# Optimization experiments

Hardware: AMD Instinct MI355X
Metric: run time of the kernel (lower is better)

The kernel has to match this reference:

```python
import jax, jax.numpy as jnp
import numpy as np

N, E, IN, HID, HEADS, OUT, G = 30000, 480000, 256, 64, 8, 128, 512
NEG_SLOPE = 0.2


def setup_inputs() -> dict:
    key = jax.random.key(0)
    ks = jax.random.split(key, 20)
    def nrm(k, shape, scale=0.05):
        return jax.random.normal(k, shape, dtype=jnp.float32) * scale
    inp = {
        'x': jax.random.normal(ks[0], (N, IN), dtype=jnp.float32),
        'edge_index': jax.random.randint(ks[1], (2, E), 0, N, dtype=jnp.int32),
        'batch': jnp.sort(jax.random.randint(ks[2], (N,), 0, G, dtype=jnp.int32)),
        # conv1: in=IN, out=HID, heads=HEADS (concat)
        'W1': nrm(ks[3], (IN, HEADS * HID)),
        'a_src1': nrm(ks[4], (HEADS, HID)),
        'a_dst1': nrm(ks[5], (HEADS, HID)),
        'b1': jnp.zeros((HEADS * HID,), jnp.float32),
        # conv2: in=HEADS*HID, out=HID, heads=HEADS (concat)
        'W2': nrm(ks[6], (HEADS * HID, HEADS * HID)),
        'a_src2': nrm(ks[7], (HEADS, HID)),
        'a_dst2': nrm(ks[8], (HEADS, HID)),
        'b2': jnp.zeros((HEADS * HID,), jnp.float32),
        # conv3: in=HEADS*HID, out=HID, heads=1
        'W3': nrm(ks[9], (HEADS * HID, HID)),
        'a_src3': nrm(ks[10], (1, HID)),
        'a_dst3': nrm(ks[11], (1, HID)),
        'b3': jnp.zeros((HID,), jnp.float32),
        # fc
        'Wfc': nrm(ks[12], (HID, OUT)),
        'bfc': jnp.zeros((OUT,), jnp.float32),
    }
    return inp


def gat_conv(x, W, a_src, a_dst, b, src, dst, heads, ch):
    # x: [N, in] -> h: [N, heads, ch]
    h = (x @ W).reshape(N, heads, ch)
    alpha_s = jnp.einsum('nhc,hc->nh', h, a_src)  # [N,H]
    alpha_d = jnp.einsum('nhc,hc->nh', h, a_dst)
    e = jax.nn.leaky_relu(alpha_s[src] + alpha_d[dst], NEG_SLOPE)  # [E',H]
    # segment softmax over incoming edges of each dst node
    e = e - jax.ops.segment_max(e, dst, num_segments=N)[dst]
    e = jnp.exp(e)
    alpha = e / jax.ops.segment_sum(e, dst, num_segments=N)[dst]
    msg = h[src] * alpha[:, :, None]                   # [E',H,C]
    out = jax.ops.segment_sum(msg, dst, num_segments=N)  # [N,H,C]
    return out.reshape(N, heads * ch) + b


def reference(x, edge_index, batch, W1, a_src1, a_dst1, b1, W2, a_src2, a_dst2, b2,
              W3, a_src3, a_dst3, b3, Wfc, bfc):
    # PyG GATConv adds self-loops
    loops = jnp.arange(N, dtype=edge_index.dtype)
    src = jnp.concatenate([edge_index[0], loops])
    dst = jnp.concatenate([edge_index[1], loops])

    h = jax.nn.elu(gat_conv(x, W1, a_src1, a_dst1, b1, src, dst, HEADS, HID))
    h = jax.nn.elu(gat_conv(h, W2, a_src2, a_dst2, b2, src, dst, HEADS, HID))
    h = jax.nn.elu(gat_conv(h, W3, a_src3, a_dst3, b3, src, dst, 1, HID))

    # global mean pool over graphs
    sums = jax.ops.segment_sum(h, batch, num_segments=G)          # [G,HID]
    cnt = jax.ops.segment_sum(jnp.ones((N,), h.dtype), batch, num_segments=G)
    pooled = sums / jnp.maximum(cnt, 1.0)[:, None]
    # dropout(p=0.5) is identity in eval mode
    return pooled @ Wfc + bfc  # [G, OUT]
```

## Files before the change

kernel.cpp:

```cpp
#include <hip/hip_runtime.h>
#include <hip/hip_fp16.h>
#include <math.h>

#define N_NODES 30000
#define N_EDGES 480000
#define N_EDGES_SL (N_EDGES + N_NODES)
#define DIM_IN 256
#define F1 512
#define HEADS 8
#define NGRAPH 512
#define NEG 0.2f
#define MB_TILES 235
#define NB_SCAN 118

typedef __attribute__((ext_vector_type(8))) short short8;
typedef __attribute__((ext_vector_type(8))) _Float16 half8;
typedef __attribute__((ext_vector_type(4))) float f32x4;

__device__ __forceinline__ float lrelu(float x) { return fmaxf(x, NEG * x); }
__device__ __forceinline__ float elu_(float x) { return x > 0.f ? x : __expf(x) - 1.f; }

__device__ __forceinline__ void glds16(const unsigned short* g, unsigned short* l) {
    __builtin_amdgcn_global_load_lds(
        (const __attribute__((address_space(1))) unsigned int*)g,
        (__attribute__((address_space(3))) unsigned int*)l, 16, 0, 0);
}

__global__ __launch_bounds__(256) void k_bsum(const int* __restrict__ deg,
                                              int* __restrict__ bsum) {
    int i = blockIdx.x * 256 + threadIdx.x;
    int v = (i < N_NODES) ? deg[i] + 1 : 0;
#pragma unroll
    for (int off = 1; off < 64; off <<= 1) v += __shfl_xor(v, off);
    __shared__ int ws[4];
    if ((threadIdx.x & 63) == 0) ws[threadIdx.x >> 6] = v;
    __syncthreads();
    if (threadIdx.x == 0) bsum[blockIdx.x] = ws[0] + ws[1] + ws[2] + ws[3];
}

__global__ __launch_bounds__(128) void k_bscan(const int* __restrict__ bsum,
                                               int* __restrict__ bbase,
                                               int* __restrict__ offsN) {
    __shared__ int p[128];
    int t = threadIdx.x;
    int v = (t < NB_SCAN) ? bsum[t] : 0;
    p[t] = v;
    __syncthreads();
    for (int off = 1; off < 128; off <<= 1) {
        int x = (t >= off) ? p[t - off] : 0;
        __syncthreads();
        p[t] += x;
        __syncthreads();
    }
    if (t < NB_SCAN) bbase[t] = p[t] - v;
    if (t == 127) *offsN = p[127];
}

__global__ __launch_bounds__(256) void k_offs(const int* __restrict__ deg,
                                              const int* __restrict__ bbase,
                                              int* __restrict__ offs,
                                              int* __restrict__ cursor) {
    int b = blockIdx.x, t = threadIdx.x;
    int i = b * 256 + t;
    int v = (i < N_NODES) ? deg[i] + 1 : 0;
    __shared__ int p[256];
    p[t] = v;
    __syncthreads();
    for (int off = 1; off < 256; off <<= 1) {
        int x = (t >= off) ? p[t - off] : 0;
        __syncthreads();
        p[t] += x;
        __syncthreads();
    }
    if (i < N_NODES) {
        int excl = bbase[b] + p[t] - v;
        offs[i] = excl;
        cursor[i] = excl;
    }
}

__global__ void k_scatter(const int* __restrict__ ei, int* __restrict__ cursor,
                          int* __restrict__ csrc) {
    int i = blockIdx.x * blockDim.x + threadIdx.x;
    if (i >= N_EDGES_SL) return;
    int s, d;
    if (i < N_EDGES) { s = ei[i]; d = ei[N_EDGES + i]; }
    else { s = d = i - N_EDGES; }
    int p = atomicAdd(&cursor[d], 1);
    csrc[p] = s;
}

__device__ __forceinline__ void d_packA(int t, const float* __restrict__ A,
                                        unsigned short* __restrict__ out,
                                        int M, int K) {
    int KB = K >> 5;
    int k8 = t & 3;
    int ml = (t >> 2) & 127;
    int tmp = t >> 9;
    int kb = tmp % KB;
    int mb = tmp / KB;
    int m = mb * 128 + ml;
    int k0 = kb * 32 + k8 * 8;
    float v[8] = {0.f, 0.f, 0.f, 0.f, 0.f, 0.f, 0.f, 0.f};
    if (m < M) {
        float4 p0 = *(const float4*)(A + (size_t)m * K + k0);
        float4 p1 = *(const float4*)(A + (size_t)m * K + k0 + 4);
        v[0] = p0.x; v[1] = p0.y; v[2] = p0.z; v[3] = p0.w;
        v[4] = p1.x; v[5] = p1.y; v[6] = p1.z; v[7] = p1.w;
    }
    unsigned short h[8];
#pragma unroll
    for (int j = 0; j < 8; ++j) h[j] = __half_as_ushort(__float2half(v[j]));
    *(short8*)(out + (size_t)t * 8) = *(short8*)h;
}

__device__ __forceinline__ void d_packW(int t, const float* __restrict__ W,
                                        unsigned short* __restrict__ out,
                                        int K, int Nn, int BN, int LB) {
    int KB = K >> 5;
    int k8 = t & 3;
    int tmp = t >> 2;
    int nl = tmp & (BN - 1);
    int tmp2 = tmp >> LB;
    int kb = tmp2 % KB;
    int nb = tmp2 / KB;
    int n = nb * BN + nl;
    int k0 = kb * 32 + k8 * 8;
    unsigned short h[8];
#pragma unroll
    for (int j = 0; j < 8; ++j)
        h[j] = __half_as_ushort(__float2half(W[(size_t)(k0 + j) * Nn + n]));
    *(short8*)(out + (size_t)t * 8) = *(short8*)h;
}

#define PB_A 3760
#define PB_W1 64
#define PB_W2 128
#define PB_W3 16
#define PB_B 118
#define PB_CNT 1875
__global__ __launch_bounds__(256) void k_packall(
        const float* __restrict__ x, const float* __restrict__ W1,
        const float* __restrict__ W2, const float* __restrict__ W3,
        const int* __restrict__ batch, const int* __restrict__ ei,
        unsigned short* __restrict__ Ah,
        unsigned short* __restrict__ Wh1, unsigned short* __restrict__ Wh2,
        unsigned short* __restrict__ Wh3, int* __restrict__ gstart,
        int* __restrict__ deg) {
    int b = blockIdx.x, tid = threadIdx.x;
    if (b < PB_A) {
        d_packA(b * 256 + tid, x, Ah, N_NODES, DIM_IN);
    } else if (b < PB_A + PB_W1) {
        d_packW((b - PB_A) * 256 + tid, W1, Wh1, DIM_IN, F1, 128, 7);
    } else if (b < PB_A + PB_W1 + PB_W2) {
        d_packW((b - PB_A - PB_W1) * 256 + tid, W2, Wh2, F1, F1, 128, 7);
    } else if (b < PB_A + PB_W1 + PB_W2 + PB_W3) {
        d_packW((b - PB_A - PB_W1 - PB_W2) * 256 + tid, W3, Wh3, F1, 64, 64, 6);
    } else if (b < PB_A + PB_W1 + PB_W2 + PB_W3 + PB_B) {
        int bb = b - (PB_A + PB_W1 + PB_W2 + PB_W3);
        int i = bb * 256 + tid;
        if (i >= N_NODES) return;
        int bt = batch[i];
        int pb = (i == 0) ? -1 : batch[i - 1];
        for (int g = pb + 1; g <= bt; ++g) gstart[g] = i;
        if (i == N_NODES - 1)
            for (int g = bt + 1; g <= NGRAPH; ++g) gstart[g] = N_NODES;
    } else {
        int i = (b - (PB_A + PB_W1 + PB_W2 + PB_W3 + PB_B)) * 256 + tid;
        if (i < N_EDGES) atomicAdd(&deg[ei[N_EDGES + i]], 1);
    }
}
#define PACKALL_BLOCKS (PB_A + PB_W1 + PB_W2 + PB_W3 + PB_B + PB_CNT)

template <int KB>
__global__ __launch_bounds__(256) void k_gemm8(const unsigned short* __restrict__ Ah,
                                               const unsigned short* __restrict__ Bh,
                                               const float* __restrict__ a_src,
                                               const float* __restrict__ a_dst,
                                               __half* __restrict__ Hf,
                                               float* __restrict__ as_,
                                               float* __restrict__ ad_,
                                               int M) {
    __shared__ unsigned short sA[4096], sB[4096];
    const int tid = threadIdx.x, lane = tid & 63, wave = tid >> 6;
    const int mb = blockIdx.x, nb = blockIdx.y;
    const int wm = (wave >> 1) * 64;
    const int wn = (wave & 1) * 64;
    const int fr = lane & 15, quad = lane >> 4;

    const unsigned short* pA = Ah + (size_t)mb * KB * 4096;
    const unsigned short* pB = Bh + (size_t)nb * KB * 4096;

    f32x4 acc[4][4];
#pragma unroll
    for (int i = 0; i < 4; ++i)
#pragma unroll
        for (int j = 0; j < 4; ++j) acc[i][j] = {0.f, 0.f, 0.f, 0.f};

    for (int kb = 0; kb < KB; ++kb) {
        const unsigned short* a_g = pA + kb * 4096;
        const unsigned short* b_g = pB + kb * 4096;
#pragma unroll
        for (int s = 0; s < 2; ++s) {
            int sg = wave * 2 + s;
            glds16(a_g + sg * 512 + lane * 8, &sA[sg * 512]);
            glds16(b_g + sg * 512 + lane * 8, &sB[sg * 512]);
        }
        __syncthreads();

        half8 af[4], bf[4];
#pragma unroll
        for (int f = 0; f < 4; ++f) {
            int m = wm + f * 16 + fr;
            af[f] = *(const half8*)&sA[m * 32 + quad * 8];
            int n = wn + f * 16 + fr;
            bf[f] = *(const half8*)&sB[n * 32 + quad * 8];
        }
#pragma unroll
        for (int i = 0; i < 4; ++i)
#pragma unroll
            for (int j = 0; j < 4; ++j)
                acc[i][j] = __builtin_amdgcn_mfma_f32_16x16x32_f16(af[i], bf[j], acc[i][j], 0, 0, 0);
        __syncthreads();
    }
    const int head = (nb * 128 + wn) >> 6;
    float avs[4], avd[4];
#pragma unroll
    for (int j = 0; j < 4; ++j) {
        avs[j] = a_src[head * 64 + j * 16 + fr];
        avd[j] = a_dst[head * 64 + j * 16 + fr];
    }
    __half* Hh = Hf + (size_t)head * N_NODES * 64;
#pragma unroll
    for (int i = 0; i < 4; ++i) {
#pragma unroll
        for (int r = 0; r < 4; ++r) {
            int row = mb * 128 + wm + i * 16 + quad * 4 + r;
            bool ok = row < M;
            float vs = 0.f, vd = 0.f;
#pragma unroll
            for (int j = 0; j < 4; ++j) {
                float c = acc[i][j][r];
                vs = fmaf(c, avs[j], vs);
                vd = fmaf(c, avd[j], vd);
                if (ok) Hh[(size_t)row * 64 + j * 16 + fr] = __float2half(c);
            }
#pragma unroll
            for (int off = 1; off < 16; off <<= 1) {
                vs += __shfl_xor(vs, off);
                vd += __shfl_xor(vd, off);
            }
            if (ok && fr == 0) {
                as_[head * N_NODES + row] = vs;
                ad_[head * N_NODES + row] = vd;
            }
        }
    }
}

template <int KB>
__global__ __launch_bounds__(256) void k_gemm1(const unsigned short* __restrict__ Ah,
                                               const unsigned short* __restrict__ Bh,
                                               const float* __restrict__ a_src,
                                               const float* __restrict__ a_dst,
                                               __half* __restrict__ C,
                                               float* __restrict__ as_,
                                               float* __restrict__ ad_,
                                               int M) {
    __shared__ unsigned short sA[4096], sB[2048];
    const int tid = threadIdx.x, lane = tid & 63, wave = tid >> 6;
    const int mb = blockIdx.x;
    const int wm = (wave >> 1) * 64;
    const int wn = (wave & 1) * 32;
    const int fr = lane & 15, quad = lane >> 4;

    const unsigned short* pA = Ah + (size_t)mb * KB * 4096;

    f32x4 acc[4][2];
#pragma unroll
    for (int i = 0; i < 4; ++i)
#pragma unroll
        for (int j = 0; j < 2; ++j) acc[i][j] = {0.f, 0.f, 0.f, 0.f};

    for (int kb = 0; kb < KB; ++kb) {
        const unsigned short* a_g = pA + kb * 4096;
        const unsigned short* b_g = Bh + kb * 2048;
#pragma unroll
        for (int s = 0; s < 2; ++s) {
            int sg = wave * 2 + s;
            glds16(a_g + sg * 512 + lane * 8, &sA[sg * 512]);
        }
        glds16(b_g + wave * 512 + lane * 8, &sB[wave * 512]);
        __syncthreads();

        half8 af[4], bf[2];
#pragma unroll
        for (int f = 0; f < 4; ++f) {
            int m = wm + f * 16 + fr;
            af[f] = *(const half8*)&sA[m * 32 + quad * 8];
        }
#pragma unroll
        for (int f = 0; f < 2; ++f) {
            int n = wn + f * 16 + fr;
            bf[f] = *(const half8*)&sB[n * 32 + quad * 8];
        }
#pragma unroll
        for (int i = 0; i < 4; ++i)
#pragma unroll
            for (int j = 0; j < 2; ++j)
                acc[i][j] = __builtin_amdgcn_mfma_f32_16x16x32_f16(af[i], bf[j], acc[i][j], 0, 0, 0);
        __syncthreads();
    }
    float avs[2], avd[2];
#pragma unroll
    for (int j = 0; j < 2; ++j) {
        avs[j] = a_src[wn + j * 16 + fr];
        avd[j] = a_dst[wn + j * 16 + fr];
    }
    float* ps = (float*)sA;
    float* pd = (float*)sB;
#pragma unroll
    for (int i = 0; i < 4; ++i) {
#pragma unroll
        for (int r = 0; r < 4; ++r) {
            int rl = wm + i * 16 + quad * 4 + r;
            int row = mb * 128 + rl;
            bool ok = row < M;
            float vs = 0.f, vd = 0.f;
#pragma unroll
            for (int j = 0; j < 2; ++j) {
                float c = acc[i][j][r];
                vs = fmaf(c, avs[j], vs);
                vd = fmaf(c, avd[j], vd);
                if (ok) C[(size_t)row * 64 + wn + j * 16 + fr] = __float2half(c);
            }
#pragma unroll
            for (int off = 1; off < 16; off <<= 1) {
                vs += __shfl_xor(vs, off);
                vd += __shfl_xor(vd, off);
            }
            if (fr == 0) {
                ps[wave * 64 + (rl & 63)] = vs;
                pd[wave * 64 + (rl & 63)] = vd;
            }
        }
    }
    __syncthreads();
    if (tid < 128) {
        int row = mb * 128 + tid;
        if (row < M) {
            int wp = (tid >> 6) * 2;
            as_[row] = ps[wp * 64 + (tid & 63)] + ps[(wp + 1) * 64 + (tid & 63)];
            ad_[row] = pd[wp * 64 + (tid & 63)] + pd[(wp + 1) * 64 + (tid & 63)];
        }
    }
}

__device__ __forceinline__ void edge_fma(float w, uint4 u, float* a) {
    const _Float16* hp = (const _Float16*)&u;
#pragma unroll
    for (int k = 0; k < 8; ++k) a[k] = fmaf(w, (float)hp[k], a[k]);
}

__global__ __launch_bounds__(256) void k_agg8(const __half* __restrict__ Hf,
                                              const float* __restrict__ as_,
                                              const float* __restrict__ ad_,
                                              const int* __restrict__ offs,
                                              const int* __restrict__ csrc,
                                              const float* __restrict__ bias,
                                              unsigned short* __restrict__ outA) {
    const int head = blockIdx.x & 7;
    const int bg = blockIdx.x >> 3;
    const int wave = threadIdx.x >> 6, lane = threadIdx.x & 63;
    const int g = lane >> 3, cl = lane & 7;
    const unsigned coff = (unsigned)(cl * 8);
    const __half* Hh = Hf + (size_t)head * N_NODES * 64;
    const float* ash = as_ + head * N_NODES;
    const float* adh = ad_ + head * N_NODES;
    float bia[8];
#pragma unroll
    for (int j = 0; j < 8; ++j) bia[j] = bias[head * 64 + cl * 8 + j];

    for (int d0 = (bg * 4 + wave) * 8; d0 < N_NODES; d0 += 8192) {
        int dst = d0 + g;
        int beg = offs[dst], end = offs[dst + 1];
        float adv = adh[dst];
        const int* cp = csrc + beg;
        int deg = end - beg;
        float s = 0.f;
        float a[8] = {0.f, 0.f, 0.f, 0.f, 0.f, 0.f, 0.f, 0.f};
        float b[8] = {0.f, 0.f, 0.f, 0.f, 0.f, 0.f, 0.f, 0.f};
        int loc = 0;
        unsigned i0 = 0, i1 = 0, i2 = 0, i3 = 0;
        if (deg >= 4) {
            i0 = (unsigned)cp[0]; i1 = (unsigned)cp[1];
            i2 = (unsigned)cp[2]; i3 = (unsigned)cp[3];
        }
        for (; loc + 3 < deg; loc += 4) {
            float e0 = ash[i0], e1 = ash[i1], e2 = ash[i2], e3 = ash[i3];
            uint4 u0 = *(const uint4*)(Hh + i0 * 64u + coff);
            uint4 u1 = *(const uint4*)(Hh + i1 * 64u + coff);
            uint4 u2 = *(const uint4*)(Hh + i2 * 64u + coff);
            uint4 u3 = *(const uint4*)(Hh + i3 * 64u + coff);
            i0 = (unsigned)cp[loc + 4]; i1 = (unsigned)cp[loc + 5];
            i2 = (unsigned)cp[loc + 6]; i3 = (unsigned)cp[loc + 7];
            float w0 = __expf(lrelu(e0 + adv));
            float w1 = __expf(lrelu(e1 + adv));
            float w2 = __expf(lrelu(e2 + adv));
            float w3 = __expf(lrelu(e3 + adv));
            s += (w0 + w1) + (w2 + w3);
            edge_fma(w0, u0, a);
            edge_fma(w1, u1, b);
            edge_fma(w2, u2, a);
            edge_fma(w3, u3, b);
        }
        for (; loc < deg; ++loc) {
            unsigned s0 = (unsigned)cp[loc];
            float w = __expf(lrelu(ash[s0] + adv));
            uint4 u = *(const uint4*)(Hh + s0 * 64u + coff);
            s += w;
            edge_fma(w, u, a);
        }
        float inv = 1.f / s;
        unsigned short h[8];
#pragma unroll
        for (int k = 0; k < 8; ++k)
            h[k] = __half_as_ushort(__float2half(elu_((a[k] + b[k]) * inv + bia[k])));
        int c0 = head * 64 + cl * 8;
        int kb = c0 >> 5, kl = c0 & 31;
        int mb = dst >> 7, ml = dst & 127;
        size_t oo = (((size_t)(mb * 16 + kb) * 128 + ml) * 32 + kl);
        *(short8*)(outA + oo) = *(short8*)h;
    }
}

__global__ __launch_bounds__(256) void k_agg1(const __half* __restrict__ Hf,
                                              const float* __restrict__ as_,
                                              const float* __restrict__ ad_,
                                              const int* __restrict__ offs,
                                              const int* __restrict__ csrc,
                                              const float* __restrict__ bias,
                                              float* __restrict__ h3) {
    const int wave = threadIdx.x >> 6, lane = threadIdx.x & 63;
    const int g = lane >> 3, cl = lane & 7;
    const unsigned coff = (unsigned)(cl * 8);
    int d0 = (blockIdx.x * 4 + wave) * 8;
    if (d0 >= N_NODES) return;
    int dst = d0 + g;
    float bia[8];
#pragma unroll
    for (int j = 0; j < 8; ++j) bia[j] = bias[cl * 8 + j];
    int beg = offs[dst], end = offs[dst + 1];
    float adv = ad_[dst];
    const int* cp = csrc + beg;
    int deg = end - beg;
    float s = 0.f;
    float a[8] = {0.f, 0.f, 0.f, 0.f, 0.f, 0.f, 0.f, 0.f};
    float b[8] = {0.f, 0.f, 0.f, 0.f, 0.f, 0.f, 0.f, 0.f};
    int loc = 0;
    unsigned i0 = 0, i1 = 0, i2 = 0, i3 = 0;
    if (deg >= 4) {
        i0 = (unsigned)cp[0]; i1 = (unsigned)cp[1];
        i2 = (unsigned)cp[2]; i3 = (unsigned)cp[3];
    }
    for (; loc + 3 < deg; loc += 4) {
        float e0 = as_[i0], e1 = as_[i1], e2 = as_[i2], e3 = as_[i3];
        uint4 u0 = *(const uint4*)(Hf + i0 * 64u + coff);
        uint4 u1 = *(const uint4*)(Hf + i1 * 64u + coff);
        uint4 u2 = *(const uint4*)(Hf + i2 * 64u + coff);
        uint4 u3 = *(const uint4*)(Hf + i3 * 64u + coff);
        i0 = (unsigned)cp[loc + 4]; i1 = (unsigned)cp[loc + 5];
        i2 = (unsigned)cp[loc + 6]; i3 = (unsigned)cp[loc + 7];
        float w0 = __expf(lrelu(e0 + adv));
        float w1 = __expf(lrelu(e1 + adv));
        float w2 = __expf(lrelu(e2 + adv));
        float w3 = __expf(lrelu(e3 + adv));
        s += (w0 + w1) + (w2 + w3);
        edge_fma(w0, u0, a);
        edge_fma(w1, u1, b);
        edge_fma(w2, u2, a);
        edge_fma(w3, u3, b);
    }
    for (; loc < deg; ++loc) {
        unsigned s0 = (unsigned)cp[loc];
        float w = __expf(lrelu(as_[s0] + adv));
        uint4 u = *(const uint4*)(Hf + s0 * 64u + coff);
        s += w;
        edge_fma(w, u, a);
    }
    float inv = 1.f / s;
    float o[8];
#pragma unroll
    for (int k = 0; k < 8; ++k) o[k] = elu_((a[k] + b[k]) * inv + bia[k]);
    float* op = h3 + (size_t)dst * 64 + cl * 8;
    *(float4*)op = make_float4(o[0], o[1], o[2], o[3]);
    *(float4*)(op + 4) = make_float4(o[4], o[5], o[6], o[7]);
}

__global__ __launch_bounds__(128) void k_poolfc(const float* __restrict__ h3,
                                                const int* __restrict__ gstart,
                                                const float* __restrict__ W,
                                                const float* __restrict__ b,
                                                float* __restrict__ out) {
    int g = blockIdx.x;
    int t = threadIdx.x;
    int s0 = gstart[g], s1 = gstart[g + 1];
    int c = t & 63, half = t >> 6;
    float acc = 0.f;
    for (int r = s0 + half; r < s1; r += 2) acc += h3[(size_t)r * 64 + c];
    __shared__ float p2[128];
    __shared__ float p[64];
    p2[t] = acc;
    __syncthreads();
    if (t < 64) {
        float cntf = (float)(s1 - s0);
        p[t] = (p2[t] + p2[t + 64]) / fmaxf(cntf, 1.f);
    }
    __syncthreads();
    float o = b[t];
#pragma unroll
    for (int k = 0; k < 64; ++k) o = fmaf(p[k], W[k * 128 + t], o);
    out[g * 128 + t] = o;
}

extern "C" void kernel_launch(void* const* d_in, const int* in_sizes, int n_in,
                              void* d_out, int out_size, void* d_ws, size_t ws_size,
                              hipStream_t stream) {
    const float* x     = (const float*)d_in[0];
    const int*   ei    = (const int*)d_in[1];
    const int*   batch = (const int*)d_in[2];
    const float* W1    = (const float*)d_in[3];
    const float* as1   = (const float*)d_in[4];
    const float* ad1   = (const float*)d_in[5];
    const float* b1    = (const float*)d_in[6];
    const float* W2    = (const float*)d_in[7];
    const float* as2   = (const float*)d_in[8];
    const float* ad2   = (const float*)d_in[9];
    const float* b2    = (const float*)d_in[10];
    const float* W3    = (const float*)d_in[11];
    const float* as3   = (const float*)d_in[12];
    const float* ad3   = (const float*)d_in[13];
    const float* b3    = (const float*)d_in[14];
    const float* Wfc   = (const float*)d_in[15];
    const float* bfc   = (const float*)d_in[16];
    float* out = (float*)d_out;

    char* ws = (char*)d_ws;
    size_t off = 0;
    auto alloc = [&](size_t bytes) -> void* {
        void* p = ws + off;
        off += (bytes + 255) & ~(size_t)255;
        return p;
    };
    __half* Hf = (__half*)alloc((size_t)HEADS * N_NODES * 64 * 2);
    __half* Hf3 = (__half*)alloc((size_t)N_NODES * 64 * 2);
    float* h3 = (float*)alloc((size_t)N_NODES * 64 * 4);
    unsigned short* Ah = (unsigned short*)alloc((size_t)MB_TILES * 16 * 4096 * 2);
    unsigned short* Wh1 = (unsigned short*)alloc((size_t)131072 * 2);
    unsigned short* Wh2 = (unsigned short*)alloc((size_t)262144 * 2);
    unsigned short* Wh3 = (unsigned short*)alloc((size_t)32768 * 2);
    float* asb   = (float*)alloc((size_t)HEADS * N_NODES * 4);
    float* adb   = (float*)alloc((size_t)HEADS * N_NODES * 4);
    int*   offs  = (int*)alloc((N_NODES + 1) * 4);
    int*   deg   = (int*)alloc(N_NODES * 4);
    int*   csrc  = (int*)alloc((size_t)N_EDGES_SL * 4 + 32);
    int*   bsum  = (int*)alloc(NB_SCAN * 4);
    int*   bbase = (int*)alloc(NB_SCAN * 4);
    int*   gstart= (int*)alloc((NGRAPH + 1) * 4);

    hipMemsetAsync(deg, 0, N_NODES * 4, stream);

    k_packall<<<PACKALL_BLOCKS, 256, 0, stream>>>(x, W1, W2, W3, batch, ei, Ah,
                                                  Wh1, Wh2, Wh3, gstart, deg);
    k_bsum<<<NB_SCAN, 256, 0, stream>>>(deg, bsum);
    k_bscan<<<1, 128, 0, stream>>>(bsum, bbase, offs + N_NODES);
    k_offs<<<NB_SCAN, 256, 0, stream>>>(deg, bbase, offs, deg);
    k_scatter<<<(N_EDGES_SL + 255) / 256, 256, 0, stream>>>(ei, deg, csrc);

    k_gemm8<8><<<dim3(MB_TILES, 4), 256, 0, stream>>>(Ah, Wh1, as1, ad1, Hf, asb, adb, N_NODES);
    k_agg8<<<2048, 256, 0, stream>>>(Hf, asb, adb, offs, csrc, b1, Ah);

    k_gemm8<16><<<dim3(MB_TILES, 4), 256, 0, stream>>>(Ah, Wh2, as2, ad2, Hf, asb, adb, N_NODES);
    k_agg8<<<2048, 256, 0, stream>>>(Hf, asb, adb, offs, csrc, b2, Ah);

    k_gemm1<16><<<MB_TILES, 256, 0, stream>>>(Ah, Wh3, as3, ad3, Hf3, asb, adb, N_NODES);
    k_agg1<<<940, 256, 0, stream>>>(Hf3, asb, adb, offs, csrc, b3, h3);

    k_poolfc<<<NGRAPH, 128, 0, stream>>>(h3, gstart, Wfc, bfc, out);
}
```

Before: 379.3 us.

## Pad CSR rows to multiples of four with 16-bit indices and vector loads

Stores CSR source indices as 16-bit values and pads each destination's adjacency list to a multiple of four, encoding the pad count in the low bits of the offset. The aggregation kernels then read indices four at a time with ushort4 loads and drop the scalar tail loop, masking padded slots through zero weights. The agg8 grid now assigns one destination group per wave instead of grid-striding. This cuts index bandwidth and per-edge branching, in exchange for padding writes in k_offs, wasted gathers on padded slots, and a hard limit of 65535 nodes.

```diff
diff --git a/kernel.cpp b/kernel.cpp
--- a/kernel.cpp
+++ b/kernel.cpp
@@ -5,6 +5,7 @@
 #define N_NODES 30000
 #define N_EDGES 480000
 #define N_EDGES_SL (N_EDGES + N_NODES)
+#define CSRC_CAP (N_EDGES + 4 * N_NODES)
 #define DIM_IN 256
 #define F1 512
 #define HEADS 8
@@ -26,10 +27,12 @@
         (__attribute__((address_space(3))) unsigned int*)l, 16, 0, 0);
 }
 
+__device__ __forceinline__ int plen_of(int deg) { return (deg + 4) & ~3; }
+
 __global__ __launch_bounds__(256) void k_bsum(const int* __restrict__ deg,
                                               int* __restrict__ bsum) {
     int i = blockIdx.x * 256 + threadIdx.x;
-    int v = (i < N_NODES) ? deg[i] + 1 : 0;
+    int v = (i < N_NODES) ? plen_of(deg[i]) : 0;
 #pragma unroll
     for (int off = 1; off < 64; off <<= 1) v += __shfl_xor(v, off);
     __shared__ int ws[4];
@@ -59,10 +62,12 @@
 __global__ __launch_bounds__(256) void k_offs(const int* __restrict__ deg,
                                               const int* __restrict__ bbase,
                                               int* __restrict__ offs,
-                                              int* __restrict__ cursor) {
+                                              int* __restrict__ cursor,
+                                              unsigned short* __restrict__ csrc) {
     int b = blockIdx.x, t = threadIdx.x;
     int i = b * 256 + t;
-    int v = (i < N_NODES) ? deg[i] + 1 : 0;
+    int d1 = 0, v = 0;
+    if (i < N_NODES) { d1 = deg[i] + 1; v = (d1 + 3) & ~3; }
     __shared__ int p[256];
     p[t] = v;
     __syncthreads();
@@ -74,20 +79,21 @@
     }
     if (i < N_NODES) {
         int excl = bbase[b] + p[t] - v;
-        offs[i] = excl;
+        offs[i] = excl | (v - d1);
         cursor[i] = excl;
+        for (int pp = excl + d1; pp < excl + v; ++pp) csrc[pp] = 0;
     }
 }
 
 __global__ void k_scatter(const int* __restrict__ ei, int* __restrict__ cursor,
-                          int* __restrict__ csrc) {
+                          unsigned short* __restrict__ csrc) {
     int i = blockIdx.x * blockDim.x + threadIdx.x;
     if (i >= N_EDGES_SL) return;
     int s, d;
     if (i < N_EDGES) { s = ei[i]; d = ei[N_EDGES + i]; }
     else { s = d = i - N_EDGES; }
     int p = atomicAdd(&cursor[d], 1);
-    csrc[p] = s;
+    csrc[p] = (unsigned short)s;
 }
 
 __device__ __forceinline__ void d_packA(int t, const float* __restrict__ A,
@@ -366,7 +372,7 @@
                                               const float* __restrict__ as_,
                                               const float* __restrict__ ad_,
                                               const int* __restrict__ offs,
-                                              const int* __restrict__ csrc,
+                                              const unsigned short* __restrict__ csrc,
                                               const float* __restrict__ bias,
                                               unsigned short* __restrict__ outA) {
     const int head = blockIdx.x & 7;
@@ -377,68 +383,79 @@
     const __half* Hh = Hf + (size_t)head * N_NODES * 64;
     const float* ash = as_ + head * N_NODES;
     const float* adh = ad_ + head * N_NODES;
+
+    int d0 = (bg * 4 + wave) * 8;
+    if (d0 >= N_NODES) return;
+    int dst = d0 + g;
+
     float bia[8];
 #pragma unroll
     for (int j = 0; j < 8; ++j) bia[j] = bias[head * 64 + cl * 8 + j];
 
-    for (int d0 = (bg * 4 + wave) * 8; d0 < N_NODES; d0 += 8192) {
-        int dst = d0 + g;
-        int beg = offs[dst], end = offs[dst + 1];
-        float adv = adh[dst];
-        const int* cp = csrc + beg;
-        int deg = end - beg;
-        float s = 0.f;
-        float a[8] = {0.f, 0.f, 0.f, 0.f, 0.f, 0.f, 0.f, 0.f};
-        float b[8] = {0.f, 0.f, 0.f, 0.f, 0.f, 0.f, 0.f, 0.f};
-        int loc = 0;
-        unsigned i0 = 0, i1 = 0, i2 = 0, i3 = 0;
-        if (deg >= 4) {
-            i0 = (unsigned)cp[0]; i1 = (unsigned)cp[1];
-            i2 = (unsigned)cp[2]; i3 = (unsigned)cp[3];
-        }
-        for (; loc + 3 < deg; loc += 4) {
-            float e0 = ash[i0], e1 = ash[i1], e2 = ash[i2], e3 = ash[i3];
-            uint4 u0 = *(const uint4*)(Hh + i0 * 64u + coff);
-            uint4 u1 = *(const uint4*)(Hh + i1 * 64u + coff);
-            uint4 u2 = *(const uint4*)(Hh + i2 * 64u + coff);
-            uint4 u3 = *(const uint4*)(Hh + i3 * 64u + coff);
-            i0 = (unsigned)cp[loc + 4]; i1 = (unsigned)cp[loc + 5];
-            i2 = (unsigned)cp[loc + 6]; i3 = (unsigned)cp[loc + 7];
-            float w0 = __expf(lrelu(e0 + adv));
-            float w1 = __expf(lrelu(e1 + adv));
-            float w2 = __expf(lrelu(e2 + adv));
-            float w3 = __expf(lrelu(e3 + adv));
-            s += (w0 + w1) + (w2 + w3);
-            edge_fma(w0, u0, a);
-            edge_fma(w1, u1, b);
-            edge_fma(w2, u2, a);
-            edge_fma(w3, u3, b);
-        }
-        for (; loc < deg; ++loc) {
-            unsigned s0 = (unsigned)cp[loc];
-            float w = __expf(lrelu(ash[s0] + adv));
-            uint4 u = *(const uint4*)(Hh + s0 * 64u + coff);
-            s += w;
-            edge_fma(w, u, a);
-        }
-        float inv = 1.f / s;
-        unsigned short h[8];
-#pragma unroll
-        for (int k = 0; k < 8; ++k)
-            h[k] = __half_as_ushort(__float2half(elu_((a[k] + b[k]) * inv + bia[k])));
-        int c0 = head * 64 + cl * 8;
-        int kb = c0 >> 5, kl = c0 & 31;
-        int mb = dst >> 7, ml = dst & 127;
-        size_t oo = (((size_t)(mb * 16 + kb) * 128 + ml) * 32 + kl);
-        *(short8*)(outA + oo) = *(short8*)h;
-    }
+    int raw0 = offs[dst], raw1 = offs[dst + 1];
+    int beg = raw0 & ~3;
+    int plen = (raw1 & ~3) - beg;
+    int nreal = 4 - (raw0 & 3);
+    float adv = adh[dst];
+    const unsigned short* cp = csrc + beg;
+
+    float s = 0.f;
+    float a[8] = {0.f, 0.f, 0.f, 0.f, 0.f, 0.f, 0.f, 0.f};
+    float b[8] = {0.f, 0.f, 0.f, 0.f, 0.f, 0.f, 0.f, 0.f};
+    ushort4 idx = *(const ushort4*)cp;
+    int loc = 0;
+    for (; loc < plen - 4; loc += 4) {
+        unsigned i0 = idx.x, i1 = idx.y, i2 = idx.z, i3 = idx.w;
+        float e0 = ash[i0], e1 = ash[i1], e2 = ash[i2], e3 = ash[i3];
+        uint4 u0 = *(const uint4*)(Hh + i0 * 64u + coff);
+        uint4 u1 = *(const uint4*)(Hh + i1 * 64u + coff);
+        uint4 u2 = *(const uint4*)(Hh + i2 * 64u + coff);
+        uint4 u3 = *(const uint4*)(Hh + i3 * 64u + coff);
+        idx = *(const ushort4*)(cp + loc + 4);
+        float w0 = __expf(lrelu(e0 + adv));
+        float w1 = __expf(lrelu(e1 + adv));
+        float w2 = __expf(lrelu(e2 + adv));
+        float w3 = __expf(lrelu(e3 + adv));
+        s += (w0 + w1) + (w2 + w3);
+        edge_fma(w0, u0, a);
+        edge_fma(w1, u1, b);
+        edge_fma(w2, u2, a);
+        edge_fma(w3, u3, b);
+    }
+    {
+        unsigned i0 = idx.x, i1 = idx.y, i2 = idx.z, i3 = idx.w;
+        float e0 = ash[i0], e1 = ash[i1], e2 = ash[i2], e3 = ash[i3];
+        uint4 u0 = *(const uint4*)(Hh + i0 * 64u + coff);
+        uint4 u1 = *(const uint4*)(Hh + i1 * 64u + coff);
+        uint4 u2 = *(const uint4*)(Hh + i2 * 64u + coff);
+        uint4 u3 = *(const uint4*)(Hh + i3 * 64u + coff);
+        float w0 = __expf(lrelu(e0 + adv));
+        float w1 = (nreal > 1) ? __expf(lrelu(e1 + adv)) : 0.f;
+        float w2 = (nreal > 2) ? __expf(lrelu(e2 + adv)) : 0.f;
+        float w3 = (nreal > 3) ? __expf(lrelu(e3 + adv)) : 0.f;
+        s += (w0 + w1) + (w2 + w3);
+        edge_fma(w0, u0, a);
+        edge_fma(w1, u1, b);
+        edge_fma(w2, u2, a);
+        edge_fma(w3, u3, b);
+    }
+    float inv = 1.f / s;
+    unsigned short h[8];
+#pragma unroll
+    for (int k = 0; k < 8; ++k)
+        h[k] = __half_as_ushort(__float2half(elu_((a[k] + b[k]) * inv + bia[k])));
+    int c0 = head * 64 + cl * 8;
+    int kb = c0 >> 5, kl = c0 & 31;
+    int mb = dst >> 7, ml = dst & 127;
+    size_t oo = (((size_t)(mb * 16 + kb) * 128 + ml) * 32 + kl);
+    *(short8*)(outA + oo) = *(short8*)h;
 }
 
 __global__ __launch_bounds__(256) void k_agg1(const __half* __restrict__ Hf,
                                               const float* __restrict__ as_,
                                               const float* __restrict__ ad_,
                                               const int* __restrict__ offs,
-                                              const int* __restrict__ csrc,
+                                              const unsigned short* __restrict__ csrc,
                                               const float* __restrict__ bias,
                                               float* __restrict__ h3) {
     const int wave = threadIdx.x >> 6, lane = threadIdx.x & 63;
@@ -450,27 +467,27 @@
     float bia[8];
 #pragma unroll
     for (int j = 0; j < 8; ++j) bia[j] = bias[cl * 8 + j];
-    int beg = offs[dst], end = offs[dst + 1];
+
+    int raw0 = offs[dst], raw1 = offs[dst + 1];
+    int beg = raw0 & ~3;
+    int plen = (raw1 & ~3) - beg;
+    int nreal = 4 - (raw0 & 3);
     float adv = ad_[dst];
-    const int* cp = csrc + beg;
-    int deg = end - beg;
+    const unsigned short* cp = csrc + beg;
+
     float s = 0.f;
     float a[8] = {0.f, 0.f, 0.f, 0.f, 0.f, 0.f, 0.f, 0.f};
     float b[8] = {0.f, 0.f, 0.f, 0.f, 0.f, 0.f, 0.f, 0.f};
+    ushort4 idx = *(const ushort4*)cp;
     int loc = 0;
-    unsigned i0 = 0, i1 = 0, i2 = 0, i3 = 0;
-    if (deg >= 4) {
-        i0 = (unsigned)cp[0]; i1 = (unsigned)cp[1];
-        i2 = (unsigned)cp[2]; i3 = (unsigned)cp[3];
-    }
-    for (; loc + 3 < deg; loc += 4) {
+    for (; loc < plen - 4; loc += 4) {
+        unsigned i0 = idx.x, i1 = idx.y, i2 = idx.z, i3 = idx.w;
         float e0 = as_[i0], e1 = as_[i1], e2 = as_[i2], e3 = as_[i3];
         uint4 u0 = *(const uint4*)(Hf + i0 * 64u + coff);
         uint4 u1 = *(const uint4*)(Hf + i1 * 64u + coff);
         uint4 u2 = *(const uint4*)(Hf + i2 * 64u + coff);
         uint4 u3 = *(const uint4*)(Hf + i3 * 64u + coff);
-        i0 = (unsigned)cp[loc + 4]; i1 = (unsigned)cp[loc + 5];
-        i2 = (unsigned)cp[loc + 6]; i3 = (unsigned)cp[loc + 7];
+        idx = *(const ushort4*)(cp + loc + 4);
         float w0 = __expf(lrelu(e0 + adv));
         float w1 = __expf(lrelu(e1 + adv));
         float w2 = __expf(lrelu(e2 + adv));
@@ -481,12 +498,22 @@
         edge_fma(w2, u2, a);
         edge_fma(w3, u3, b);
     }
-    for (; loc < deg; ++loc) {
-        unsigned s0 = (unsigned)cp[loc];
-        float w = __expf(lrelu(as_[s0] + adv));
-        uint4 u = *(const uint4*)(Hf + s0 * 64u + coff);
-        s += w;
-        edge_fma(w, u, a);
+    {
+        unsigned i0 = idx.x, i1 = idx.y, i2 = idx.z, i3 = idx.w;
+        float e0 = as_[i0], e1 = as_[i1], e2 = as_[i2], e3 = as_[i3];
+        uint4 u0 = *(const uint4*)(Hf + i0 * 64u + coff);
+        uint4 u1 = *(const uint4*)(Hf + i1 * 64u + coff);
+        uint4 u2 = *(const uint4*)(Hf + i2 * 64u + coff);
+        uint4 u3 = *(const uint4*)(Hf + i3 * 64u + coff);
+        float w0 = __expf(lrelu(e0 + adv));
+        float w1 = (nreal > 1) ? __expf(lrelu(e1 + adv)) : 0.f;
+        float w2 = (nreal > 2) ? __expf(lrelu(e2 + adv)) : 0.f;
+        float w3 = (nreal > 3) ? __expf(lrelu(e3 + adv)) : 0.f;
+        s += (w0 + w1) + (w2 + w3);
+        edge_fma(w0, u0, a);
+        edge_fma(w1, u1, b);
+        edge_fma(w2, u2, a);
+        edge_fma(w3, u3, b);
     }
     float inv = 1.f / s;
     float o[8];
@@ -563,7 +590,8 @@
     float* adb   = (float*)alloc((size_t)HEADS * N_NODES * 4);
     int*   offs  = (int*)alloc((N_NODES + 1) * 4);
     int*   deg   = (int*)alloc(N_NODES * 4);
-    int*   csrc  = (int*)alloc((size_t)N_EDGES_SL * 4 + 32);
+    int*   cursor= (int*)alloc(N_NODES * 4);
+    unsigned short* csrc = (unsigned short*)alloc((size_t)CSRC_CAP * 2 + 64);
     int*   bsum  = (int*)alloc(NB_SCAN * 4);
     int*   bbase = (int*)alloc(NB_SCAN * 4);
     int*   gstart= (int*)alloc((NGRAPH + 1) * 4);
@@ -574,14 +602,14 @@
                                                   Wh1, Wh2, Wh3, gstart, deg);
     k_bsum<<<NB_SCAN, 256, 0, stream>>>(deg, bsum);
     k_bscan<<<1, 128, 0, stream>>>(bsum, bbase, offs + N_NODES);
-    k_offs<<<NB_SCAN, 256, 0, stream>>>(deg, bbase, offs, deg);
-    k_scatter<<<(N_EDGES_SL + 255) / 256, 256, 0, stream>>>(ei, deg, csrc);
+    k_offs<<<NB_SCAN, 256, 0, stream>>>(deg, bbase, offs, cursor, csrc);
+    k_scatter<<<(N_EDGES_SL + 255) / 256, 256, 0, stream>>>(ei, cursor, csrc);
 
     k_gemm8<8><<<dim3(MB_TILES, 4), 256, 0, stream>>>(Ah, Wh1, as1, ad1, Hf, asb, adb, N_NODES);
-    k_agg8<<<2048, 256, 0, stream>>>(Hf, asb, adb, offs, csrc, b1, Ah);
+    k_agg8<<<938 * 8, 256, 0, stream>>>(Hf, asb, adb, offs, csrc, b1, Ah);
 
     k_gemm8<16><<<dim3(MB_TILES, 4), 256, 0, stream>>>(Ah, Wh2, as2, ad2, Hf, asb, adb, N_NODES);
-    k_agg8<<<2048, 256, 0, stream>>>(Hf, asb, adb, offs, csrc, b2, Ah);
+    k_agg8<<<938 * 8, 256, 0, stream>>>(Hf, asb, adb, offs, csrc, b2, Ah);
 
     k_gemm1<16><<<MB_TILES, 256, 0, stream>>>(Ah, Wh3, as3, ad3, Hf3, asb, adb, N_NODES);
     k_agg1<<<940, 256, 0, stream>>>(Hf3, asb, adb, offs, csrc, b3, h3);
```

Result: faster. 355.5 us, median of 2 (-6.3%).
